# Optimization experiments

Measured on AMD Instinct MI355X. Metric: run time of the kernel, lower is better.

Reference implementation:

```python
import jax, jax.numpy as jnp
import numpy as np

V, D, N, T, U, E = 200000, 128, 50000, 20, 128, 128

def setup_inputs() -> dict:
    key = jax.random.key(0)
    ks = jax.random.split(key, 12)
    s = 0.02
    return {
        "node_ids": jax.random.randint(ks[0], (N,), 0, V, dtype=jnp.int32),
        "neigh_ids": jax.random.randint(ks[1], (N, T), 0, V, dtype=jnp.int32),
        "alpha": jax.random.uniform(ks[2], (N, T), dtype=jnp.float32),
        "table": jax.random.normal(ks[3], (V, D), dtype=jnp.float32),
        "Wq": jax.random.normal(ks[4], (D, U), dtype=jnp.float32) * s,
        "bq": jnp.zeros((U,), dtype=jnp.float32),
        "Wn": jax.random.normal(ks[5], (D, U), dtype=jnp.float32) * s,
        "bn": jnp.zeros((U,), dtype=jnp.float32),
        "Ww": jax.random.normal(ks[6], (2 * U, U), dtype=jnp.float32) * s,
        "bw": jnp.zeros((U,), dtype=jnp.float32),
        "Wg": jax.random.normal(ks[7], (U, E), dtype=jnp.float32) * s,
        "bg": jnp.zeros((E,), dtype=jnp.float32),
    }

def reference(node_ids, neigh_ids, alpha, table, Wq, bq, Wn, bn, Ww, bw, Wg, bg):
    # gather initial embeddings (irregular indexing)
    node_x = table[node_ids]            # [N, D]
    neigh_x = table[neigh_ids]          # [N, T, D]
    # Convolve: node branch Dense+ReLU
    node_h = jax.nn.relu(node_x @ Wq + bq)                       # [N, U]
    # Aggregator: neighbor Dense+ReLU then alpha-weighted matmul
    neigh_h = jax.nn.relu(jnp.einsum('ntd,du->ntu', neigh_x, Wn) + bn)  # [N, T, U]
    agg = jnp.einsum('nt,ntu->nu', alpha, neigh_h)               # [N, U]
    # concat + Dense+ReLU
    emb = jax.nn.relu(jnp.concatenate([node_h, agg], axis=-1) @ Ww + bw)  # [N, U]
    # global (Frobenius) L2 normalize, as in tf.divide(Emb, tf.norm(Emb, ord=2))
    emb = emb / jnp.linalg.norm(emb)
    # final Dense+ReLU to emb_dim
    return jax.nn.relu(emb @ Wg + bg)                            # [N, E]
```

## Files before the change

### kernel.cpp

```cpp
#include <hip/hip_runtime.h>
#include <math.h>


using f32x4  = __attribute__((ext_vector_type(4))) float;
using short8 = __attribute__((ext_vector_type(8))) short;

__device__ __forceinline__ ushort f2bf(float f) {
    uint u = __float_as_uint(f);
    return (ushort)((u + 0x7fffu + ((u >> 16) & 1u)) >> 16);
}
__device__ __forceinline__ float bf2f(ushort h) {
    return __uint_as_float((uint)h << 16);
}
__device__ __forceinline__ uint pk2(float lo, float hi) {
    return (uint)f2bf(lo) | ((uint)f2bf(hi) << 16);
}

__global__ __launch_bounds__(256)
void prep_weights(const float* __restrict__ Wq, const float* __restrict__ Wn,
                  const float* __restrict__ Ww, const float* __restrict__ Wg,
                  ushort* __restrict__ WqT, ushort* __restrict__ WnT,
                  ushort* __restrict__ WwT, ushort* __restrict__ WgT)
{
    int idx = blockIdx.x * 256 + threadIdx.x;
    const float* W; ushort* WT; int K; int j = idx;
    if (j < 16384)      { W = Wq; WT = WqT; K = 128; }
    else if (j < 32768) { W = Wn; WT = WnT; K = 128; j -= 16384; }
    else if (j < 65536) { W = Ww; WT = WwT; K = 256; j -= 32768; }
    else                { W = Wg; WT = WgT; K = 128; j -= 65536; }
    int n = j & 127, k = j >> 7;
    WT[(size_t)n * K + k] = f2bf(W[j]);
}

__device__ __forceinline__ void stage_w128(const ushort* __restrict__ WT,
                                           const float* __restrict__ bias,
                                           ushort* Wlds, float* blds, int tid)
{
#pragma unroll
    for (int it = 0; it < 8; ++it) {
        int idx = it * 256 + tid, n = idx >> 4, o = idx & 15;
        uint4 v = *reinterpret_cast<const uint4*>(&WT[(size_t)n * 128 + 8 * o]);
        *reinterpret_cast<uint4*>((char*)Wlds + n * 256 + ((16 * o) ^ ((n & 7) << 4))) = v;
    }
    if (tid < 128) blds[tid] = bias[tid];
}

template<bool GATHER>
__device__ __forceinline__ void k1_side(const float* __restrict__ table,
                                        const int* __restrict__ gidx,
                                        const ushort* Wlds, const float* blds,
                                        ushort* Albs,
                                        ushort* __restrict__ out, int ldo, int M,
                                        int sideIdx, int sideBlk)
{
    const int tid = threadIdx.x;
    const int w = tid >> 6, l = tid & 63, l16 = l & 15, lh = l >> 4;
    const int nt = (M + 63) >> 6;
    int tile = sideIdx;

    f32x4 f[8];
    if (tile < nt) {
#pragma unroll
        for (int j = 0; j < 8; ++j) {
            int u = j * 256 + tid;
            int r = u >> 5, c4 = u & 31;
            int row = tile * 64 + r;
            int g = (row < M) ? row : (M - 1);
            if (GATHER) g = gidx[g];
            f[j] = *reinterpret_cast<const f32x4*>(table + (size_t)g * 128 + 4 * c4);
        }
    }
    __syncthreads();

    for (; tile < nt; tile += sideBlk) {
        uint2 p[8];
#pragma unroll
        for (int j = 0; j < 8; ++j) {
            p[j].x = pk2(f[j][0], f[j][1]);
            p[j].y = pk2(f[j][2], f[j][3]);
        }
        __syncthreads();
#pragma unroll
        for (int j = 0; j < 8; ++j) {
            int u = j * 256 + tid, r = u >> 5, c4 = u & 31;
            *reinterpret_cast<uint2*>(
                (char*)Albs + r * 256 + ((8 * c4) ^ ((r & 7) << 4))) = p[j];
        }
        __syncthreads();

        const int nxt = tile + sideBlk;
        if (nxt < nt) {
#pragma unroll
            for (int j = 0; j < 8; ++j) {
                int u = j * 256 + tid;
                int r = u >> 5, c4 = u & 31;
                int row = nxt * 64 + r;
                int g = (row < M) ? row : (M - 1);
                if (GATHER) g = gidx[g];
                f[j] = *reinterpret_cast<const f32x4*>(table + (size_t)g * 128 + 4 * c4);
            }
        }

        f32x4 acc[8];
#pragma unroll
        for (int mt = 0; mt < 8; ++mt)
#pragma unroll
            for (int i = 0; i < 4; ++i) acc[mt][i] = 0.f;
        const int r0 = 16 * w + l16;
#pragma unroll
        for (int ks = 0; ks < 4; ++ks) {
            short8 a = *reinterpret_cast<const short8*>(
                (const char*)Albs + r0 * 256 + ((64 * ks + 16 * lh) ^ ((r0 & 7) << 4)));
#pragma unroll
            for (int mt = 0; mt < 8; ++mt) {
                short8 wf = *reinterpret_cast<const short8*>(
                    (const char*)Wlds + (16 * mt + l16) * 256 +
                    ((64 * ks + 16 * lh) ^ ((l16 & 7) << 4)));
                acc[mt] = __builtin_amdgcn_mfma_f32_16x16x32_bf16(wf, a, acc[mt], 0, 0, 0);
            }
        }

        const int row = tile * 64 + r0;
        if (row < M) {
#pragma unroll
            for (int mt = 0; mt < 8; ++mt) {
                f32x4 bv = *reinterpret_cast<const f32x4*>(&blds[16 * mt + 4 * lh]);
                uint2 q;
                q.x = pk2(fmaxf(acc[mt][0] + bv[0], 0.f), fmaxf(acc[mt][1] + bv[1], 0.f));
                q.y = pk2(fmaxf(acc[mt][2] + bv[2], 0.f), fmaxf(acc[mt][3] + bv[3], 0.f));
                *reinterpret_cast<uint2*>(&out[(size_t)row * ldo + 16 * mt + 4 * lh]) = q;
            }
        }
    }
}

__global__ __launch_bounds__(256, 3)
void k1_dual(const float* __restrict__ table, const int* __restrict__ node_ids,
             const ushort* __restrict__ WnT, const float* __restrict__ bn,
             const ushort* __restrict__ WqT, const float* __restrict__ bq,
             ushort* __restrict__ H, ushort* __restrict__ nh,
             int V, int N, int splitH, int nBlk)
{
    __shared__ __align__(16) ushort Wlds[128 * 128];
    __shared__ __align__(16) ushort Albs[64 * 128];
    __shared__ __align__(16) float blds[128];
    const int tid = threadIdx.x;
    const bool isH = (int)blockIdx.x < splitH;

    stage_w128(isH ? WnT : WqT, isH ? bn : bq, Wlds, blds, tid);

    if (isH)
        k1_side<false>(table, nullptr, Wlds, blds, Albs, H, 128, V,
                       blockIdx.x, splitH);
    else
        k1_side<true>(table, node_ids, Wlds, blds, Albs, nh, 256, N,
                      blockIdx.x - splitH, nBlk - splitH);
}

__global__ __launch_bounds__(256)
void agg_bf16(const ushort* __restrict__ H,
              const int* __restrict__ nids,
              const float* __restrict__ alpha,
              ushort* __restrict__ outb,
              int N)
{
    const int n   = blockIdx.x * 16 + (threadIdx.x >> 4);
    const int l16 = threadIdx.x & 15;
    if (n >= N) return;

    const int*   idp = &nids[n * 20];
    const float* alp = &alpha[n * 20];
    float a[8];
#pragma unroll
    for (int j = 0; j < 8; ++j) a[j] = 0.f;
#pragma unroll
    for (int t = 0; t < 20; ++t) {
        const int   id = idp[t];
        const float al = alp[t];
        uint4 h = *reinterpret_cast<const uint4*>(&H[(size_t)id * 128 + 8 * l16]);
        a[0] = fmaf(al, bf2f((ushort)(h.x & 0xffff)), a[0]);
        a[1] = fmaf(al, bf2f((ushort)(h.x >> 16)),    a[1]);
        a[2] = fmaf(al, bf2f((ushort)(h.y & 0xffff)), a[2]);
        a[3] = fmaf(al, bf2f((ushort)(h.y >> 16)),    a[3]);
        a[4] = fmaf(al, bf2f((ushort)(h.z & 0xffff)), a[4]);
        a[5] = fmaf(al, bf2f((ushort)(h.z >> 16)),    a[5]);
        a[6] = fmaf(al, bf2f((ushort)(h.w & 0xffff)), a[6]);
        a[7] = fmaf(al, bf2f((ushort)(h.w >> 16)),    a[7]);
    }
    uint4 p;
    p.x = pk2(a[0], a[1]); p.y = pk2(a[2], a[3]);
    p.z = pk2(a[4], a[5]); p.w = pk2(a[6], a[7]);
    *reinterpret_cast<uint4*>(&outb[(size_t)n * 256 + 8 * l16]) = p;
}

template<int KTOT, bool GATHER, bool ABF16, bool SUMSQ, bool SCALE, bool OUTBF16>
__global__ __launch_bounds__(256, 2)
void mfma_gemm(const void* __restrict__ Av, int lda,
               const int* __restrict__ gidx,
               const ushort* __restrict__ WT,
               const float* __restrict__ bias,
               void* __restrict__ outv, int ldo, int M,
               float* __restrict__ partials,
               const float* __restrict__ scale_ptr)
{
    __shared__ __align__(16) char smem[65536];
    __shared__ float red[256];
    char* Bbase = smem + 32768;

    const int tid = threadIdx.x;
    const int w   = tid >> 6;
    const int l   = tid & 63;
    const int l16 = l & 15, lh = l >> 4;
    const int brow = blockIdx.x * 128;

    f32x4 acc[2][8];
#pragma unroll
    for (int fr = 0; fr < 2; ++fr)
#pragma unroll
        for (int fc = 0; fc < 8; ++fc)
#pragma unroll
            for (int i = 0; i < 4; ++i) acc[fr][fc][i] = 0.f;

    for (int k0 = 0; k0 < KTOT; k0 += 128) {
        if (ABF16) {
            const ushort* A = (const ushort*)Av;
#pragma unroll
            for (int it = 0; it < 8; ++it) {
                int idx = it * 256 + tid;
                int r = idx >> 4, o = idx & 15;
                int row = brow + r; int grow = (row < M) ? row : (M - 1);
                if (GATHER) grow = gidx[grow];
                uint4 v = *reinterpret_cast<const uint4*>(&A[(size_t)grow * lda + k0 + 8 * o]);
                *reinterpret_cast<uint4*>(smem + r * 256 + ((16 * o) ^ ((r & 7) << 4))) = v;
            }
        } else {
            const float* A = (const float*)Av;
#pragma unroll
            for (int it = 0; it < 16; ++it) {
                int idx = it * 256 + tid;
                int r = idx >> 5, q = idx & 31;
                int row = brow + r; int grow = (row < M) ? row : (M - 1);
                if (GATHER) grow = gidx[grow];
                float4 v = *reinterpret_cast<const float4*>(&A[(size_t)grow * lda + k0 + 4 * q]);
                uint2 p;
                p.x = pk2(v.x, v.y);
                p.y = pk2(v.z, v.w);
                *reinterpret_cast<uint2*>(smem + r * 256 + ((8 * q) ^ ((r & 7) << 4))) = p;
            }
        }
#pragma unroll
        for (int it = 0; it < 8; ++it) {
            int idx = it * 256 + tid;
            int n = idx >> 4, o = idx & 15;
            uint4 v = *reinterpret_cast<const uint4*>(&WT[(size_t)n * KTOT + k0 + 8 * o]);
            *reinterpret_cast<uint4*>(Bbase + n * 256 + ((16 * o) ^ ((n & 7) << 4))) = v;
        }
        __syncthreads();

        const int r0 = 32 * w + l16;
        const int r1 = r0 + 16;
#pragma unroll
        for (int ks = 0; ks < 4; ++ks) {
            const int kb = 64 * ks + 16 * lh;
            short8 a0 = *reinterpret_cast<const short8*>(
                smem + r0 * 256 + (kb ^ ((r0 & 7) << 4)));
            short8 a1 = *reinterpret_cast<const short8*>(
                smem + r1 * 256 + (kb ^ ((r1 & 7) << 4)));
#pragma unroll
            for (int fc = 0; fc < 8; ++fc) {
                const int nn = 16 * fc + l16;
                short8 b = *reinterpret_cast<const short8*>(
                    Bbase + nn * 256 + (kb ^ ((nn & 7) << 4)));
                acc[0][fc] = __builtin_amdgcn_mfma_f32_16x16x32_bf16(a0, b, acc[0][fc], 0, 0, 0);
                acc[1][fc] = __builtin_amdgcn_mfma_f32_16x16x32_bf16(a1, b, acc[1][fc], 0, 0, 0);
            }
        }
        __syncthreads();
    }

    const float scale = SCALE ? scale_ptr[0] : 1.0f;
    float bloc[8];
#pragma unroll
    for (int fc = 0; fc < 8; ++fc) bloc[fc] = bias[16 * fc + l16];

    float ssq = 0.f;
#pragma unroll
    for (int fr = 0; fr < 2; ++fr)
#pragma unroll
        for (int fc = 0; fc < 8; ++fc)
#pragma unroll
            for (int i = 0; i < 4; ++i) {
                const int r   = 32 * w + 16 * fr + 4 * lh + i;
                const int col = 16 * fc + l16;
                float v = fmaxf(fmaf(acc[fr][fc][i], scale, bloc[fc]), 0.f);
                if (SUMSQ) { if (brow + r < M) ssq += v * v; }
                if (OUTBF16) ((ushort*)smem)[r * 128 + col] = f2bf(v);
                else         ((float*)smem)[r * 128 + col] = v;
            }
    __syncthreads();

    if (OUTBF16) {
        ushort* out = (ushort*)outv;
#pragma unroll
        for (int it = 0; it < 8; ++it) {
            int idx = it * 256 + tid;
            int r = idx >> 4, o = idx & 15;
            if (brow + r < M)
                *reinterpret_cast<uint4*>(&out[(size_t)(brow + r) * ldo + 8 * o]) =
                    *reinterpret_cast<const uint4*>((ushort*)smem + r * 128 + 8 * o);
        }
    } else {
        float* out = (float*)outv;
#pragma unroll
        for (int it = 0; it < 16; ++it) {
            int idx = it * 256 + tid;
            int r = idx >> 5, q = idx & 31;
            if (brow + r < M)
                *reinterpret_cast<float4*>(&out[(size_t)(brow + r) * ldo + 4 * q]) =
                    *reinterpret_cast<const float4*>((float*)smem + r * 128 + 4 * q);
        }
    }

    if (SUMSQ) {
        red[tid] = ssq;
        __syncthreads();
        for (int st = 128; st > 0; st >>= 1) {
            if (tid < st) red[tid] += red[tid + st];
            __syncthreads();
        }
        if (tid == 0) partials[blockIdx.x] = red[0];
    }
}

__global__ void reduce_norm(const float* __restrict__ partials, int n,
                            float* __restrict__ scale)
{
    __shared__ float red[256];
    float s = 0.f;
    for (int i = threadIdx.x; i < n; i += 256) s += partials[i];
    red[threadIdx.x] = s;
    __syncthreads();
    for (int st = 128; st > 0; st >>= 1) {
        if (threadIdx.x < st) red[threadIdx.x] += red[threadIdx.x + st];
        __syncthreads();
    }
    if (threadIdx.x == 0) scale[0] = 1.0f / sqrtf(red[0]);
}

extern "C" void kernel_launch(void* const* d_in, const int* in_sizes, int n_in,
                              void* d_out, int out_size, void* d_ws, size_t ws_size,
                              hipStream_t stream)
{
    const int*   node_ids  = (const int*)  d_in[0];
    const int*   neigh_ids = (const int*)  d_in[1];
    const float* alpha     = (const float*)d_in[2];
    const float* table     = (const float*)d_in[3];
    const float* Wq        = (const float*)d_in[4];
    const float* bq        = (const float*)d_in[5];
    const float* Wn        = (const float*)d_in[6];
    const float* bn        = (const float*)d_in[7];
    const float* Ww        = (const float*)d_in[8];
    const float* bw        = (const float*)d_in[9];
    const float* Wg        = (const float*)d_in[10];
    const float* bg        = (const float*)d_in[11];

    const int N = in_sizes[0];
    const int V = in_sizes[3] / 128;
    float* out = (float*)d_out;

    ushort* H    = (ushort*)d_ws;
    ushort* nh   = H    + (size_t)V * 128;
    ushort* embb = nh   + (size_t)N * 256;
    ushort* WqT  = embb + (size_t)N * 128;
    ushort* WnT  = WqT  + 16384;
    ushort* WwT  = WnT  + 16384;
    ushort* WgT  = WwT  + 32768;
    float*  partials = (float*)(WgT + 16384);
    float*  scale    = partials + 512;

    const size_t need = (size_t)((char*)(scale + 16) - (char*)d_ws);
    if (ws_size < need) return;

    const int nblkN = (N + 127) / 128;

    const int G1 = 768;
    const long long tH = (V + 63) / 64, tN = (N + 63) / 64;
    int splitH = (int)((G1 * tH) / (tH + tN));
    if (splitH < 1) splitH = 1;
    if (splitH > G1 - 1) splitH = G1 - 1;

    prep_weights<<<320, 256, 0, stream>>>(Wq, Wn, Ww, Wg, WqT, WnT, WwT, WgT);
    k1_dual<<<G1, 256, 0, stream>>>(table, node_ids, WnT, bn, WqT, bq,
                                    H, nh, V, N, splitH, G1);
    agg_bf16<<<(N + 15) / 16, 256, 0, stream>>>(H, neigh_ids, alpha, nh + 128, N);
    mfma_gemm<256, false, true, true, false, true><<<nblkN, 256, 0, stream>>>(
        nh, 256, nullptr, WwT, bw, embb, 128, N, partials, nullptr);
    reduce_norm<<<1, 256, 0, stream>>>(partials, nblkN, scale);
    mfma_gemm<128, false, true, false, true, false><<<nblkN, 256, 0, stream>>>(
        embb, 128, nullptr, WgT, bg, out, 128, N, nullptr, scale);
}
```

Baseline: 103.7 us.

## Double-buffer table rows into LDS via async global_load_lds in first GEMM

Replaces the register-prefetch plus bf16-pack-to-LDS staging of table rows with direct global-to-LDS async loads (global_load_lds) into a double-buffered fp32 LDS tile. The bf16 conversion moves to after the LDS read, right before the MFMA. Tiles shrink to 32 rows, blocks to 128 threads, and the grid to 512. The aim is to remove register pressure and the extra sync/pack stage so loads overlap compute, at the cost of more LDS per block and lower per-block parallelism.

```diff
diff --git a/kernel.cpp b/kernel.cpp
--- a/kernel.cpp
+++ b/kernel.cpp
@@ -4,6 +4,13 @@
 
 using f32x4  = __attribute__((ext_vector_type(4))) float;
 using short8 = __attribute__((ext_vector_type(8))) short;
+
+typedef const void __attribute__((address_space(1))) gvoid_t;
+typedef void       __attribute__((address_space(3))) svoid_t;
+
+__device__ __forceinline__ void gload16(const void* g, void* l) {
+    __builtin_amdgcn_global_load_lds((gvoid_t*)g, (svoid_t*)l, 16, 0, 0);
+}
 
 __device__ __forceinline__ ushort f2bf(float f) {
     uint u = __float_as_uint(f);
@@ -14,6 +21,12 @@
 }
 __device__ __forceinline__ uint pk2(float lo, float hi) {
     return (uint)f2bf(lo) | ((uint)f2bf(hi) << 16);
+}
+__device__ __forceinline__ short8 pack8(f32x4 a, f32x4 b) {
+    uint4 r;
+    r.x = pk2(a[0], a[1]); r.y = pk2(a[2], a[3]);
+    r.z = pk2(b[0], b[1]); r.w = pk2(b[2], b[3]);
+    union { uint4 u; short8 s; } cv; cv.u = r; return cv.s;
 }
 
 __global__ __launch_bounds__(256)
@@ -32,73 +45,82 @@
     WT[(size_t)n * K + k] = f2bf(W[j]);
 }
 
-__device__ __forceinline__ void stage_w128(const ushort* __restrict__ WT,
-                                           const float* __restrict__ bias,
-                                           ushort* Wlds, float* blds, int tid)
-{
-#pragma unroll
-    for (int it = 0; it < 8; ++it) {
-        int idx = it * 256 + tid, n = idx >> 4, o = idx & 15;
+template<bool GATHER>
+__device__ __forceinline__ void stage_tile(const float* __restrict__ table,
+                                           const int* __restrict__ gidx,
+                                           float* Ab, int tile, int M,
+                                           int w, int l)
+{
+#pragma unroll
+    for (int j = 0; j < 8; ++j) {
+        const int u   = j * 2 + w;
+        const int idx = u * 64 + l;
+        const int r   = idx >> 5;
+        const int c   = idx & 31;
+        int grow = tile * 32 + r;
+        if (grow > M - 1) grow = M - 1;
+        const int g = GATHER ? gidx[grow] : grow;
+        const char* src = (const char*)table + (size_t)g * 512
+                        + (size_t)((c * 16) ^ ((r & 7) << 4));
+        gload16(src, (char*)Ab + u * 1024);
+    }
+}
+
+__global__ __launch_bounds__(128, 2)
+void k1_async(const float* __restrict__ table, const int* __restrict__ node_ids,
+              const ushort* __restrict__ WnT, const float* __restrict__ bn,
+              const ushort* __restrict__ WqT, const float* __restrict__ bq,
+              ushort* __restrict__ H, ushort* __restrict__ nh,
+              int V, int N, int splitH)
+{
+    __shared__ __align__(16) ushort Wlds[128 * 128];
+    __shared__ __align__(16) float  Abuf[2][32 * 128];
+    __shared__ __align__(16) float  blds[128];
+    const int tid = threadIdx.x;
+    const int w = tid >> 6, l = tid & 63, l16 = l & 15, lh = l >> 4;
+    const bool isH = (int)blockIdx.x < splitH;
+
+    const ushort* WT = isH ? WnT : WqT;
+#pragma unroll
+    for (int it = 0; it < 16; ++it) {
+        int idx = it * 128 + tid, n = idx >> 4, o = idx & 15;
         uint4 v = *reinterpret_cast<const uint4*>(&WT[(size_t)n * 128 + 8 * o]);
         *reinterpret_cast<uint4*>((char*)Wlds + n * 256 + ((16 * o) ^ ((n & 7) << 4))) = v;
     }
-    if (tid < 128) blds[tid] = bias[tid];
-}
-
-template<bool GATHER>
-__device__ __forceinline__ void k1_side(const float* __restrict__ table,
-                                        const int* __restrict__ gidx,
-                                        const ushort* Wlds, const float* blds,
-                                        ushort* Albs,
-                                        ushort* __restrict__ out, int ldo, int M,
-                                        int sideIdx, int sideBlk)
-{
-    const int tid = threadIdx.x;
-    const int w = tid >> 6, l = tid & 63, l16 = l & 15, lh = l >> 4;
-    const int nt = (M + 63) >> 6;
-    int tile = sideIdx;
-
-    f32x4 f[8];
+    blds[tid] = (isH ? bn : bq)[tid];
+
+    const int M   = isH ? V : N;
+    ushort* out   = isH ? H : nh;
+    const int ldo = isH ? 128 : 256;
+    const int nt  = (M + 31) >> 5;
+    const int bidx = isH ? (int)blockIdx.x : (int)blockIdx.x - splitH;
+    const int nblk = isH ? splitH : (int)gridDim.x - splitH;
+
+    int tile = bidx;
     if (tile < nt) {
-#pragma unroll
-        for (int j = 0; j < 8; ++j) {
-            int u = j * 256 + tid;
-            int r = u >> 5, c4 = u & 31;
-            int row = tile * 64 + r;
-            int g = (row < M) ? row : (M - 1);
-            if (GATHER) g = gidx[g];
-            f[j] = *reinterpret_cast<const f32x4*>(table + (size_t)g * 128 + 4 * c4);
-        }
+        if (isH) stage_tile<false>(table, nullptr,  Abuf[0], tile, M, w, l);
+        else     stage_tile<true >(table, node_ids, Abuf[0], tile, M, w, l);
     }
     __syncthreads();
 
-    for (; tile < nt; tile += sideBlk) {
-        uint2 p[8];
-#pragma unroll
-        for (int j = 0; j < 8; ++j) {
-            p[j].x = pk2(f[j][0], f[j][1]);
-            p[j].y = pk2(f[j][2], f[j][3]);
-        }
-        __syncthreads();
-#pragma unroll
-        for (int j = 0; j < 8; ++j) {
-            int u = j * 256 + tid, r = u >> 5, c4 = u & 31;
-            *reinterpret_cast<uint2*>(
-                (char*)Albs + r * 256 + ((8 * c4) ^ ((r & 7) << 4))) = p[j];
-        }
-        __syncthreads();
-
-        const int nxt = tile + sideBlk;
+    int cur = 0;
+    const int r = 16 * w + l16;
+    for (; tile < nt; tile += nblk) {
+        const int nxt = tile + nblk;
         if (nxt < nt) {
-#pragma unroll
-            for (int j = 0; j < 8; ++j) {
-                int u = j * 256 + tid;
-                int r = u >> 5, c4 = u & 31;
-                int row = nxt * 64 + r;
-                int g = (row < M) ? row : (M - 1);
-                if (GATHER) g = gidx[g];
-                f[j] = *reinterpret_cast<const f32x4*>(table + (size_t)g * 128 + 4 * c4);
-            }
+            if (isH) stage_tile<false>(table, nullptr,  Abuf[cur ^ 1], nxt, M, w, l);
+            else     stage_tile<true >(table, node_ids, Abuf[cur ^ 1], nxt, M, w, l);
+        }
+
+        const char* Ab = (const char*)Abuf[cur];
+        short8 a[4];
+#pragma unroll
+        for (int ks = 0; ks < 4; ++ks) {
+            f32x4 b0 = *reinterpret_cast<const f32x4*>(
+                Ab + r * 512 + ((ks * 128 + lh * 32)      ^ ((r & 7) << 4)));
+            f32x4 b1 = *reinterpret_cast<const f32x4*>(
+                Ab + r * 512 + ((ks * 128 + lh * 32 + 16) ^ ((r & 7) << 4)));
+            a[ks] = pack8(b0, b1);
         }
 
         f32x4 acc[8];
@@ -106,55 +128,30 @@
         for (int mt = 0; mt < 8; ++mt)
 #pragma unroll
             for (int i = 0; i < 4; ++i) acc[mt][i] = 0.f;
-        const int r0 = 16 * w + l16;
-#pragma unroll
-        for (int ks = 0; ks < 4; ++ks) {
-            short8 a = *reinterpret_cast<const short8*>(
-                (const char*)Albs + r0 * 256 + ((64 * ks + 16 * lh) ^ ((r0 & 7) << 4)));
+#pragma unroll
+        for (int ks = 0; ks < 4; ++ks)
 #pragma unroll
             for (int mt = 0; mt < 8; ++mt) {
                 short8 wf = *reinterpret_cast<const short8*>(
                     (const char*)Wlds + (16 * mt + l16) * 256 +
                     ((64 * ks + 16 * lh) ^ ((l16 & 7) << 4)));
-                acc[mt] = __builtin_amdgcn_mfma_f32_16x16x32_bf16(wf, a, acc[mt], 0, 0, 0);
-            }
-        }
-
-        const int row = tile * 64 + r0;
-        if (row < M) {
+                acc[mt] = __builtin_amdgcn_mfma_f32_16x16x32_bf16(wf, a[ks], acc[mt], 0, 0, 0);
+            }
+
+        const int grow = tile * 32 + r;
+        if (grow < M) {
 #pragma unroll
             for (int mt = 0; mt < 8; ++mt) {
                 f32x4 bv = *reinterpret_cast<const f32x4*>(&blds[16 * mt + 4 * lh]);
                 uint2 q;
                 q.x = pk2(fmaxf(acc[mt][0] + bv[0], 0.f), fmaxf(acc[mt][1] + bv[1], 0.f));
                 q.y = pk2(fmaxf(acc[mt][2] + bv[2], 0.f), fmaxf(acc[mt][3] + bv[3], 0.f));
-                *reinterpret_cast<uint2*>(&out[(size_t)row * ldo + 16 * mt + 4 * lh]) = q;
-            }
-        }
-    }
-}
-
-__global__ __launch_bounds__(256, 3)
-void k1_dual(const float* __restrict__ table, const int* __restrict__ node_ids,
-             const ushort* __restrict__ WnT, const float* __restrict__ bn,
-             const ushort* __restrict__ WqT, const float* __restrict__ bq,
-             ushort* __restrict__ H, ushort* __restrict__ nh,
-             int V, int N, int splitH, int nBlk)
-{
-    __shared__ __align__(16) ushort Wlds[128 * 128];
-    __shared__ __align__(16) ushort Albs[64 * 128];
-    __shared__ __align__(16) float blds[128];
-    const int tid = threadIdx.x;
-    const bool isH = (int)blockIdx.x < splitH;
-
-    stage_w128(isH ? WnT : WqT, isH ? bn : bq, Wlds, blds, tid);
-
-    if (isH)
-        k1_side<false>(table, nullptr, Wlds, blds, Albs, H, 128, V,
-                       blockIdx.x, splitH);
-    else
-        k1_side<true>(table, node_ids, Wlds, blds, Albs, nh, 256, N,
-                      blockIdx.x - splitH, nBlk - splitH);
+                *reinterpret_cast<uint2*>(&out[(size_t)grow * ldo + 16 * mt + 4 * lh]) = q;
+            }
+        }
+        __syncthreads();
+        cur ^= 1;
+    }
 }
 
 __global__ __launch_bounds__(256)
@@ -383,15 +380,15 @@
 
     const int nblkN = (N + 127) / 128;
 
-    const int G1 = 768;
-    const long long tH = (V + 63) / 64, tN = (N + 63) / 64;
+    const int G1 = 512;
+    const long long tH = (V + 31) / 32, tN = (N + 31) / 32;
     int splitH = (int)((G1 * tH) / (tH + tN));
     if (splitH < 1) splitH = 1;
     if (splitH > G1 - 1) splitH = G1 - 1;
 
     prep_weights<<<320, 256, 0, stream>>>(Wq, Wn, Ww, Wg, WqT, WnT, WwT, WgT);
-    k1_dual<<<G1, 256, 0, stream>>>(table, node_ids, WnT, bn, WqT, bq,
-                                    H, nh, V, N, splitH, G1);
+    k1_async<<<G1, 128, 0, stream>>>(table, node_ids, WnT, bn, WqT, bq,
+                                     H, nh, V, N, splitH);
     agg_bf16<<<(N + 15) / 16, 256, 0, stream>>>(H, neigh_ids, alpha, nh + 128, N);
     mfma_gemm<256, false, true, true, false, true><<<nblkN, 256, 0, stream>>>(
         nh, 256, nullptr, WwT, bw, embb, 128, N, partials, nullptr);
```

Result: slower. 112.5 us (+8.5%).
